# Kernel tuning notes

Hardware: AMD Instinct MI355X
Metric: run time of the kernel (lower is better)

## Reference

```python
import jax, jax.numpy as jnp
import numpy as np

L, B, H, D, S, FF = 24, 4, 16, 512, 4096, 2048
HD = D // H
POS = 2048  # current kv_cache_len (write position)
EPS = 1e-5
SCALE = 1.0 / np.sqrt(HD)


def layer_norm(x, w, b):
    m = jnp.mean(x, axis=-1, keepdims=True)
    v = jnp.mean(jnp.square(x - m), axis=-1, keepdims=True)
    return (x - m) * jax.lax.rsqrt(v + EPS) * w + b


def setup_inputs() -> dict:
    key = jax.random.key(0)
    ks = jax.random.split(key, 12)
    f = lambda k, shape: jax.random.normal(k, shape, dtype=jnp.float32) * 0.02
    # decode mask: positions [0, POS] are attendable (index_fill_ sets POS True)
    attn_mask = jnp.broadcast_to(jnp.arange(S) <= POS, (B, H, 1, S))
    return {
        "x": jax.random.normal(ks[0], (B, 1, D), dtype=jnp.float32),
        "k_cache": jax.random.normal(ks[1], (L, B, H, S, HD), dtype=jnp.float32),
        "v_cache": jax.random.normal(ks[2], (L, B, H, S, HD), dtype=jnp.float32),
        "attn_mask": attn_mask,
        "qkv_w": f(ks[3], (L, 3 * D, D)),
        "qkv_b": f(ks[4], (L, 3 * D)),
        "out_w": f(ks[5], (L, D, D)),
        "out_b": f(ks[6], (L, D)),
        "mlp_w1": f(ks[7], (L, FF, D)),
        "mlp_b1": f(ks[8], (L, FF)),
        "mlp_w2": f(ks[9], (L, D, FF)),
        "mlp_b2": f(ks[10], (L, D)),
        "norm_w1": jnp.ones((L, D), jnp.float32),
        "norm_b1": jnp.zeros((L, D), jnp.float32),
        "norm_w2": jnp.ones((L, D), jnp.float32),
        "norm_b2": jnp.zeros((L, D), jnp.float32),
        "kv_cache_len": POS,
    }


def reference(x, k_cache, v_cache, attn_mask, qkv_w, qkv_b, out_w, out_b,
              mlp_w1, mlp_b1, mlp_w2, mlp_b2, norm_w1, norm_b1, norm_w2,
              norm_b2, kv_cache_len):
    pos = kv_cache_len

    def block(h, p):
        kc0, vc0, qw, qb, ow, ob, w1, b1, w2, b2, nw1, nb1, nw2, nb2 = p
        qkv = h @ qw.T + qb                      # [B,1,3D]
        q, k, v = jnp.split(qkv, 3, axis=-1)
        q = q.reshape(B, 1, H, HD).transpose(0, 2, 1, 3)   # [B,H,1,HD]
        k = k.reshape(B, 1, H, HD).transpose(0, 2, 1, 3)
        v = v.reshape(B, 1, H, HD).transpose(0, 2, 1, 3)
        # in-place cache update at write position (index_copy_ on dim 2)
        kc = kc0.at[:, :, pos, :].set(k[:, :, 0, :])       # [B,H,S,HD]
        vc = vc0.at[:, :, pos, :].set(v[:, :, 0, :])
        scores = jnp.einsum('bhqd,bhkd->bhqk', q, kc) * SCALE
        scores = jnp.where(attn_mask, scores, -1e9)
        attn = jnp.einsum('bhqk,bhkd->bhqd', jax.nn.softmax(scores, axis=-1), vc)
        attn = attn.transpose(0, 2, 1, 3).reshape(B, 1, D)
        attn = attn @ ow.T + ob
        h = layer_norm(h + attn, nw1, nb1)
        mlp = jax.nn.relu(h @ w1.T + b1) @ w2.T + b2
        h = layer_norm(h + mlp, nw2, nb2)
        return h, None

    xs = (k_cache, v_cache, qkv_w, qkv_b, out_w, out_b, mlp_w1, mlp_b1,
          mlp_w2, mlp_b2, norm_w1, norm_b1, norm_w2, norm_b2)
    out, _ = jax.lax.scan(block, x, xs)
    return out
```

## Files before the change

kernel.cpp:

```cpp
#include <hip/hip_runtime.h>


#define DEV __device__ __forceinline__

static constexpr int LNUM = 24;
static constexpr int B = 4;
static constexpr int H = 16;
static constexpr int D = 512;
static constexpr int S = 4096;
static constexpr int FF = 2048;
static constexpr int HD = 32;
static constexpr int NCH = 9;
static constexpr float EPS = 1e-5f;
static constexpr float SCALE = 0.17677669529663687f;

DEV float waveReduceSum(float v) {
#pragma unroll
    for (int o = 32; o > 0; o >>= 1) v += __shfl_xor(v, o);
    return v;
}
DEV float waveReduceMax(float v) {
#pragma unroll
    for (int o = 32; o > 0; o >>= 1) v = fmaxf(v, __shfl_xor(v, o));
    return v;
}
DEV float blockReduceSum(float v, float* red) {
    v = waveReduceSum(v);
    __syncthreads();
    if ((threadIdx.x & 63) == 0) red[threadIdx.x >> 6] = v;
    __syncthreads();
    return red[0] + red[1] + red[2] + red[3];
}
DEV float blockReduceMax(float v, float* red) {
    v = waveReduceMax(v);
    __syncthreads();
    if ((threadIdx.x & 63) == 0) red[threadIdx.x >> 6] = v;
    __syncthreads();
    return fmaxf(fmaxf(red[0], red[1]), fmaxf(red[2], red[3]));
}

__global__ __launch_bounds__(256) void k_qkv(
    const float* __restrict__ hsrc, int apply_ln,
    const float* __restrict__ nw, const float* __restrict__ nb,
    const float* __restrict__ w, const float* __restrict__ bias,
    float* __restrict__ qkv)
{
    const int lane = threadIdx.x & 63;
    const int wid = (blockIdx.x << 2) + (threadIdx.x >> 6);
    const int b = wid / 1536;
    const int r = wid - b * 1536;
    const float* hb = hsrc + (b << 9);
    const int k0 = lane << 3;
    float4 h0 = *(const float4*)(hb + k0);
    float4 h1 = *(const float4*)(hb + k0 + 4);
    float hv[8] = {h0.x, h0.y, h0.z, h0.w, h1.x, h1.y, h1.z, h1.w};
    if (apply_ln) {
        float s = 0.f, s2 = 0.f;
#pragma unroll
        for (int j = 0; j < 8; ++j) { s += hv[j]; s2 += hv[j] * hv[j]; }
        s = waveReduceSum(s);
        s2 = waveReduceSum(s2);
        float mean = s * (1.f / 512.f);
        float var = s2 * (1.f / 512.f) - mean * mean;
        float rs = rsqrtf(var + EPS);
        float4 nw0 = *(const float4*)(nw + k0);
        float4 nw1 = *(const float4*)(nw + k0 + 4);
        float4 nb0 = *(const float4*)(nb + k0);
        float4 nb1 = *(const float4*)(nb + k0 + 4);
        float nwv[8] = {nw0.x, nw0.y, nw0.z, nw0.w, nw1.x, nw1.y, nw1.z, nw1.w};
        float nbv[8] = {nb0.x, nb0.y, nb0.z, nb0.w, nb1.x, nb1.y, nb1.z, nb1.w};
#pragma unroll
        for (int j = 0; j < 8; ++j) hv[j] = (hv[j] - mean) * rs * nwv[j] + nbv[j];
    }
    const float* wr = w + (size_t)r * 512 + k0;
    float4 w0 = *(const float4*)(wr);
    float4 w1 = *(const float4*)(wr + 4);
    float acc = w0.x * hv[0] + w0.y * hv[1] + w0.z * hv[2] + w0.w * hv[3]
              + w1.x * hv[4] + w1.y * hv[5] + w1.z * hv[6] + w1.w * hv[7];
    acc = waveReduceSum(acc);
    if (lane == 0) {
        float v = acc + bias[r];
        if (r < 512) v *= SCALE;
        qkv[b * 1536 + r] = v;
    }
}

__global__ __launch_bounds__(256) void k_attn(
    const float* __restrict__ kc, const float* __restrict__ vc,
    const float* __restrict__ qkv, float* __restrict__ part,
    const int* __restrict__ posp)
{
    const int tid = threadIdx.x;
    const int c = blockIdx.x % NCH;
    const int bh = blockIdx.x / NCH;
    const int b = bh >> 4, h = bh & 15;
    const int pos = posp[0];
    __shared__ float qs[32];
    __shared__ float es[256];
    __shared__ float red[4];
    __shared__ float op[8][33];
    if (tid < 32) qs[tid] = qkv[b * 1536 + h * 32 + tid];
    __syncthreads();
    float score = -1e30f;
    bool act = false;
    if (c < 8) {
        int p = c * 256 + tid;
        act = (p < pos);
        const float4* kp = (const float4*)(kc + ((size_t)bh * S + p) * HD);
        float s = 0.f;
#pragma unroll
        for (int i = 0; i < 8; ++i) {
            float4 kv = kp[i];
            s += qs[4 * i] * kv.x + qs[4 * i + 1] * kv.y + qs[4 * i + 2] * kv.z + qs[4 * i + 3] * kv.w;
        }
        if (act) score = s;
    } else if (tid == 0) {
        act = true;
        const float* kp = qkv + b * 1536 + 512 + h * 32;
        float s = 0.f;
#pragma unroll
        for (int j = 0; j < 32; ++j) s += qs[j] * kp[j];
        score = s;
    }
    float m = blockReduceMax(score, red);
    float e = act ? expf(score - m) : 0.f;
    es[tid] = e;
    float l = blockReduceSum(e, red);
    const int d = tid & 31, g = tid >> 5;
    float acc = 0.f;
    if (c < 8) {
        const float* vp = vc + ((size_t)bh * S + c * 256 + g * 32) * HD + d;
#pragma unroll 8
        for (int i = 0; i < 32; ++i) acc += es[g * 32 + i] * vp[(size_t)i * HD];
    } else if (g == 0) {
        acc = es[0] * qkv[b * 1536 + 1024 + h * 32 + d];
    }
    op[g][d] = acc;
    __syncthreads();
    if (tid < 32) {
        float o = 0.f;
#pragma unroll
        for (int gg = 0; gg < 8; ++gg) o += op[gg][tid];
        float* pp = part + (size_t)(bh * NCH + c) * 34;
        pp[2 + tid] = o;
        if (tid == 0) { pp[0] = m; pp[1] = l; }
    }
}

__global__ __launch_bounds__(256) void k_outproj(
    const float* __restrict__ part,
    const float* __restrict__ ow, const float* __restrict__ ob,
    const float* __restrict__ hsrc, int apply_ln,
    const float* __restrict__ nw, const float* __restrict__ nb,
    float* __restrict__ t1)
{
    const int tid = threadIdx.x;
    const int b = blockIdx.x >> 5;
    const int oc = blockIdx.x & 31;
    __shared__ float attn_s[512];
    __shared__ float hln[512];
    __shared__ float mh[16], sh[16];
    __shared__ float red[4];
    if (tid < 16) {
        const float* pp = part + (size_t)(b * 16 + tid) * NCH * 34;
        float m = -1e30f;
        for (int c = 0; c < NCH; ++c) m = fmaxf(m, pp[c * 34]);
        float ss = 0.f;
        for (int c = 0; c < NCH; ++c) ss += pp[c * 34 + 1] * expf(pp[c * 34] - m);
        mh[tid] = m;
        sh[tid] = ss;
    }
    __syncthreads();
#pragma unroll
    for (int e = tid; e < 512; e += 256) {
        int h = e >> 5, d = e & 31;
        const float* pp = part + (size_t)(b * 16 + h) * NCH * 34;
        float o = 0.f;
        for (int c = 0; c < NCH; ++c) o += pp[c * 34 + 2 + d] * expf(pp[c * 34] - mh[h]);
        attn_s[e] = o / sh[h];
    }
    float a0 = hsrc[(b << 9) + tid], a1 = hsrc[(b << 9) + 256 + tid];
    if (apply_ln) {
        float s = blockReduceSum(a0 + a1, red);
        float s2 = blockReduceSum(a0 * a0 + a1 * a1, red);
        float mean = s * (1.f / 512.f);
        float rs = rsqrtf(s2 * (1.f / 512.f) - mean * mean + EPS);
        hln[tid] = (a0 - mean) * rs * nw[tid] + nb[tid];
        hln[tid + 256] = (a1 - mean) * rs * nw[tid + 256] + nb[tid + 256];
    } else {
        hln[tid] = a0;
        hln[tid + 256] = a1;
    }
    __syncthreads();
    const int w = tid >> 6, lane = tid & 63, k0 = lane << 3;
#pragma unroll
    for (int oi = 0; oi < 4; ++oi) {
        int dd = (oc << 4) + (w << 2) + oi;
        const float4* wp = (const float4*)(ow + (size_t)dd * 512 + k0);
        float4 w0 = wp[0], w1 = wp[1];
        float acc = w0.x * attn_s[k0] + w0.y * attn_s[k0 + 1] + w0.z * attn_s[k0 + 2] + w0.w * attn_s[k0 + 3]
                  + w1.x * attn_s[k0 + 4] + w1.y * attn_s[k0 + 5] + w1.z * attn_s[k0 + 6] + w1.w * attn_s[k0 + 7];
        acc = waveReduceSum(acc);
        if (lane == 0) t1[(b << 9) + dd] = hln[dd] + acc + ob[dd];
    }
}

__global__ __launch_bounds__(256) void k_mlp1(
    const float* __restrict__ t1,
    const float* __restrict__ nw, const float* __restrict__ nb,
    const float* __restrict__ w1, const float* __restrict__ b1,
    float* __restrict__ m1)
{
    const int tid = threadIdx.x;
    const int b = blockIdx.x >> 7;
    const int oc = blockIdx.x & 127;
    __shared__ float hln[512];
    __shared__ float red[4];
    float a0 = t1[(b << 9) + tid], a1 = t1[(b << 9) + 256 + tid];
    float s = blockReduceSum(a0 + a1, red);
    float s2 = blockReduceSum(a0 * a0 + a1 * a1, red);
    float mean = s * (1.f / 512.f);
    float rs = rsqrtf(s2 * (1.f / 512.f) - mean * mean + EPS);
    hln[tid] = (a0 - mean) * rs * nw[tid] + nb[tid];
    hln[tid + 256] = (a1 - mean) * rs * nw[tid + 256] + nb[tid + 256];
    __syncthreads();
    const int w = tid >> 6, lane = tid & 63, k0 = lane << 3;
#pragma unroll
    for (int oi = 0; oi < 4; ++oi) {
        int r = (oc << 4) + (w << 2) + oi;
        const float4* wp = (const float4*)(w1 + (size_t)r * 512 + k0);
        float4 w0 = wp[0], w1v = wp[1];
        float acc = w0.x * hln[k0] + w0.y * hln[k0 + 1] + w0.z * hln[k0 + 2] + w0.w * hln[k0 + 3]
                  + w1v.x * hln[k0 + 4] + w1v.y * hln[k0 + 5] + w1v.z * hln[k0 + 6] + w1v.w * hln[k0 + 7];
        acc = waveReduceSum(acc);
        if (lane == 0) m1[(b << 11) + r] = fmaxf(acc + b1[r], 0.f);
    }
}

__global__ __launch_bounds__(256) void k_mlp2(
    const float* __restrict__ m1, const float* __restrict__ t1,
    const float* __restrict__ nw, const float* __restrict__ nb,
    const float* __restrict__ w2, const float* __restrict__ b2,
    float* __restrict__ sout)
{
    const int tid = threadIdx.x;
    const int b = blockIdx.x >> 7;
    const int oc = blockIdx.x & 127;
    __shared__ float ms[2048];
    __shared__ float red[4];
#pragma unroll
    for (int i = 0; i < 8; ++i) ms[tid + (i << 8)] = m1[(b << 11) + tid + (i << 8)];
    float a0 = t1[(b << 9) + tid], a1 = t1[(b << 9) + 256 + tid];
    float s = blockReduceSum(a0 + a1, red);
    float s2 = blockReduceSum(a0 * a0 + a1 * a1, red);
    float mean = s * (1.f / 512.f);
    float rs = rsqrtf(s2 * (1.f / 512.f) - mean * mean + EPS);
    const int w = tid >> 6, lane = tid & 63;
    const int dd = (oc << 2) + w;
    const float4* wp = (const float4*)(w2 + (size_t)dd * 2048);
    float acc = 0.f;
#pragma unroll
    for (int i = 0; i < 8; ++i) {
        int idx = (i << 6) + lane;
        float4 q = wp[idx];
        int k = idx << 2;
        acc += q.x * ms[k] + q.y * ms[k + 1] + q.z * ms[k + 2] + q.w * ms[k + 3];
    }
    acc = waveReduceSum(acc);
    if (lane == 0) {
        float td = t1[(b << 9) + dd];
        float hd = (td - mean) * rs * nw[dd] + nb[dd];
        sout[(b << 9) + dd] = hd + acc + b2[dd];
    }
}

__global__ __launch_bounds__(256) void k_finalln(
    const float* __restrict__ sbuf,
    const float* __restrict__ nw, const float* __restrict__ nb,
    float* __restrict__ out)
{
    const int b = blockIdx.x, tid = threadIdx.x;
    __shared__ float red[4];
    float a0 = sbuf[(b << 9) + tid], a1 = sbuf[(b << 9) + 256 + tid];
    float s = blockReduceSum(a0 + a1, red);
    float s2 = blockReduceSum(a0 * a0 + a1 * a1, red);
    float mean = s * (1.f / 512.f);
    float rs = rsqrtf(s2 * (1.f / 512.f) - mean * mean + EPS);
    out[(b << 9) + tid] = (a0 - mean) * rs * nw[tid] + nb[tid];
    out[(b << 9) + 256 + tid] = (a1 - mean) * rs * nw[tid + 256] + nb[tid + 256];
}

extern "C" void kernel_launch(void* const* d_in, const int* in_sizes, int n_in,
                              void* d_out, int out_size, void* d_ws, size_t ws_size,
                              hipStream_t stream)
{
    const float* x    = (const float*)d_in[0];
    const float* kc   = (const float*)d_in[1];
    const float* vc   = (const float*)d_in[2];
    const float* qkvw = (const float*)d_in[4];
    const float* qkvb = (const float*)d_in[5];
    const float* outw = (const float*)d_in[6];
    const float* outb = (const float*)d_in[7];
    const float* w1   = (const float*)d_in[8];
    const float* b1   = (const float*)d_in[9];
    const float* w2   = (const float*)d_in[10];
    const float* b2   = (const float*)d_in[11];
    const float* nw1  = (const float*)d_in[12];
    const float* nb1  = (const float*)d_in[13];
    const float* nw2  = (const float*)d_in[14];
    const float* nb2  = (const float*)d_in[15];
    const int*   posp = (const int*)d_in[16];

    float* ws      = (float*)d_ws;
    float* qkvbuf  = ws;
    float* part    = qkvbuf + 6144;
    float* t1      = part + 19584;
    float* m1      = t1 + 2048;
    float* sbuf    = m1 + 8192;

    const size_t kvLayerStride = (size_t)B * H * S * HD;

    for (int l = 0; l < LNUM; ++l) {
        const float* hsrc = (l == 0) ? x : sbuf;
        const int aln = (l > 0) ? 1 : 0;
        const float* pnw = (l > 0) ? (nw2 + (size_t)(l - 1) * 512) : nullptr;
        const float* pnb = (l > 0) ? (nb2 + (size_t)(l - 1) * 512) : nullptr;

        k_qkv<<<1536, 256, 0, stream>>>(hsrc, aln, pnw, pnb,
                                        qkvw + (size_t)l * 1536 * 512,
                                        qkvb + (size_t)l * 1536, qkvbuf);
        k_attn<<<B * H * NCH, 256, 0, stream>>>(kc + (size_t)l * kvLayerStride,
                                                vc + (size_t)l * kvLayerStride,
                                                qkvbuf, part, posp);
        k_outproj<<<B * 32, 256, 0, stream>>>(part,
                                              outw + (size_t)l * 512 * 512,
                                              outb + (size_t)l * 512,
                                              hsrc, aln, pnw, pnb, t1);
        k_mlp1<<<B * 128, 256, 0, stream>>>(t1,
                                            nw1 + (size_t)l * 512, nb1 + (size_t)l * 512,
                                            w1 + (size_t)l * FF * D, b1 + (size_t)l * FF, m1);
        k_mlp2<<<B * 128, 256, 0, stream>>>(m1, t1,
                                            nw1 + (size_t)l * 512, nb1 + (size_t)l * 512,
                                            w2 + (size_t)l * D * FF, b2 + (size_t)l * 512, sbuf);
    }
    k_finalln<<<B, 256, 0, stream>>>(sbuf, nw2 + 23 * 512, nb2 + 23 * 512, (float*)d_out);
}
```

Measured before the change: 820.1 us.

## Fuse all layers into one persistent cooperative kernel with grid syncs

```diff
diff --git a/kernel.cpp b/kernel.cpp
--- a/kernel.cpp
+++ b/kernel.cpp
@@ -1,4 +1,7 @@
 #include <hip/hip_runtime.h>
+#include <hip/hip_cooperative_groups.h>
+
+namespace cg = cooperative_groups;
 
 
 #define DEV __device__ __forceinline__
@@ -24,19 +27,336 @@
     for (int o = 32; o > 0; o >>= 1) v = fmaxf(v, __shfl_xor(v, o));
     return v;
 }
-DEV float blockReduceSum(float v, float* red) {
+DEV float blockReduceSum(float v, volatile float* red) {
     v = waveReduceSum(v);
     __syncthreads();
     if ((threadIdx.x & 63) == 0) red[threadIdx.x >> 6] = v;
     __syncthreads();
     return red[0] + red[1] + red[2] + red[3];
 }
-DEV float blockReduceMax(float v, float* red) {
+DEV float blockReduceMax(float v, volatile float* red) {
     v = waveReduceMax(v);
     __syncthreads();
     if ((threadIdx.x & 63) == 0) red[threadIdx.x >> 6] = v;
     __syncthreads();
     return fmaxf(fmaxf(red[0], red[1]), fmaxf(red[2], red[3]));
+}
+
+struct Params {
+    const float *x, *kc, *vc;
+    const float *qkvw, *qkvb, *outw, *outb, *w1, *b1, *w2, *b2;
+    const float *nw1, *nb1, *nw2, *nb2;
+    const int* posp;
+    float *qkvbuf, *part, *t1, *m1, *sbuf, *out;
+};
+
+__global__ __launch_bounds__(256, 2) void mega(Params p) {
+    cg::grid_group grid = cg::this_grid();
+    const int blk = blockIdx.x;
+    const int tid = threadIdx.x;
+    const int w = tid >> 6;
+    const int lane = tid & 63;
+    const int pos = p.posp[0];
+
+    __shared__ float SM[6160];
+    float* red = SM + 6152;
+
+    for (int l = 0; l < LNUM; ++l) {
+        const float* hsrc = (l == 0) ? p.x : p.sbuf;
+        const bool aln = (l > 0);
+        const float* pnw = p.nw2 + (aln ? (size_t)(l - 1) * 512 : 0);
+        const float* pnb = p.nb2 + (aln ? (size_t)(l - 1) * 512 : 0);
+        const float* qwL = p.qkvw + (size_t)l * 1536 * 512;
+        const float* qbL = p.qkvb + (size_t)l * 1536;
+        const float* kcL = p.kc + (size_t)l * 8388608;
+        const float* vcL = p.vc + (size_t)l * 8388608;
+        const float* owL = p.outw + (size_t)l * 512 * 512;
+        const float* obL = p.outb + (size_t)l * 512;
+        const float* w1L = p.w1 + (size_t)l * 2048 * 512;
+        const float* b1L = p.b1 + (size_t)l * 2048;
+        const float* w2L = p.w2 + (size_t)l * 512 * 2048;
+        const float* b2L = p.b2 + (size_t)l * 512;
+        const float* n1w = p.nw1 + (size_t)l * 512;
+        const float* n1b = p.nb1 + (size_t)l * 512;
+
+        {
+            const float4* s4 = (const float4*)hsrc;
+            float4* m4 = (float4*)SM;
+            m4[tid] = s4[tid];
+            m4[tid + 256] = s4[tid + 256];
+            __syncthreads();
+            float4* h4 = (float4*)(SM + (w << 9));
+            float4 aa = h4[lane], bb = h4[lane + 64];
+            float s = aa.x + aa.y + aa.z + aa.w + bb.x + bb.y + bb.z + bb.w;
+            float s2 = aa.x * aa.x + aa.y * aa.y + aa.z * aa.z + aa.w * aa.w
+                     + bb.x * bb.x + bb.y * bb.y + bb.z * bb.z + bb.w * bb.w;
+            s = waveReduceSum(s);
+            s2 = waveReduceSum(s2);
+            float mean = s * (1.f / 512.f);
+            float rs = rsqrtf(s2 * (1.f / 512.f) - mean * mean + EPS);
+            if (aln) {
+                const float4* gw4 = (const float4*)pnw;
+                const float4* gb4 = (const float4*)pnb;
+                float4 gw = gw4[lane], gb = gb4[lane];
+                aa.x = (aa.x - mean) * rs * gw.x + gb.x;
+                aa.y = (aa.y - mean) * rs * gw.y + gb.y;
+                aa.z = (aa.z - mean) * rs * gw.z + gb.z;
+                aa.w = (aa.w - mean) * rs * gw.w + gb.w;
+                h4[lane] = aa;
+                gw = gw4[lane + 64]; gb = gb4[lane + 64];
+                bb.x = (bb.x - mean) * rs * gw.x + gb.x;
+                bb.y = (bb.y - mean) * rs * gw.y + gb.y;
+                bb.z = (bb.z - mean) * rs * gw.z + gb.z;
+                bb.w = (bb.w - mean) * rs * gw.w + gb.w;
+                h4[lane + 64] = bb;
+            }
+            __syncthreads();
+            const int r = (blk << 2) + w;
+            if (r < 1536) {
+                const float4* wr4 = (const float4*)(qwL + (size_t)r * 512);
+                float4 wA = wr4[lane], wB = wr4[lane + 64];
+                float acc[4];
+#pragma unroll
+                for (int b = 0; b < 4; ++b) {
+                    const float4* hb4 = (const float4*)(SM + (b << 9));
+                    float4 hA = hb4[lane], hB = hb4[lane + 64];
+                    float a = wA.x * hA.x + wA.y * hA.y + wA.z * hA.z + wA.w * hA.w
+                            + wB.x * hB.x + wB.y * hB.y + wB.z * hB.z + wB.w * hB.w;
+                    acc[b] = waveReduceSum(a);
+                }
+                if (lane == 0) {
+                    float bias = qbL[r];
+                    float sc = (r < 512) ? SCALE : 1.f;
+#pragma unroll
+                    for (int b = 0; b < 4; ++b)
+                        p.qkvbuf[b * 1536 + r] = (acc[b] + bias) * sc;
+                }
+            }
+        }
+        grid.sync();
+
+        {
+            const int c = blk & 7, bh = blk >> 3;
+            const int b = bh >> 4, h = bh & 15;
+            float* qs = SM;
+            float* es = SM + 32;
+            float* op = SM + 288;
+            float* sn = SM + 560;
+            if (tid < 32) qs[tid] = p.qkvbuf[b * 1536 + h * 32 + tid];
+            __syncthreads();
+            const int pp = (c << 8) + tid;
+            const bool act = pp < pos;
+            const float4* kp = (const float4*)(kcL + ((size_t)bh * 4096 + pp) * 32);
+            float sc = 0.f;
+#pragma unroll
+            for (int i = 0; i < 8; ++i) {
+                float4 kv = kp[i];
+                sc += qs[4 * i] * kv.x + qs[4 * i + 1] * kv.y
+                    + qs[4 * i + 2] * kv.z + qs[4 * i + 3] * kv.w;
+            }
+            float score = act ? sc : -1e30f;
+            float smax = score;
+            float snew = 0.f;
+            if (c == 7 && tid == 0) {
+                const float* kn = p.qkvbuf + b * 1536 + 512 + h * 32;
+                for (int j = 0; j < 32; ++j) snew += qs[j] * kn[j];
+                smax = fmaxf(smax, snew);
+            }
+            float m = blockReduceMax(smax, red);
+            if (tid == 0) sn[0] = (c == 7) ? expf(snew - m) : 0.f;
+            float e = act ? expf(score - m) : 0.f;
+            es[tid] = e;
+            float lsum = blockReduceSum(e, red) + sn[0];
+            const int d = tid & 31, g = tid >> 5;
+            float acc = 0.f;
+            const float* vp = vcL + ((size_t)bh * 4096 + (c << 8) + (g << 5)) * 32 + d;
+#pragma unroll 8
+            for (int i = 0; i < 32; ++i) acc += es[(g << 5) + i] * vp[(size_t)i * 32];
+            if (g == 0) acc += sn[0] * p.qkvbuf[b * 1536 + 1024 + h * 32 + d];
+            op[g * 33 + d] = acc;
+            __syncthreads();
+            if (tid < 32) {
+                float o = 0.f;
+#pragma unroll
+                for (int gg = 0; gg < 8; ++gg) o += op[gg * 33 + tid];
+                float* pt = p.part + (size_t)((bh << 3) + c) * 34;
+                pt[2 + tid] = o;
+                if (tid == 0) { pt[0] = m; pt[1] = lsum; }
+            }
+        }
+        grid.sync();
+
+        {
+            const float4* s4 = (const float4*)hsrc;
+            float4* m4 = (float4*)SM;
+            m4[tid] = s4[tid];
+            m4[tid + 256] = s4[tid + 256];
+            __syncthreads();
+            float4* h4 = (float4*)(SM + (w << 9));
+            float4 aa = h4[lane], bb = h4[lane + 64];
+            float s = aa.x + aa.y + aa.z + aa.w + bb.x + bb.y + bb.z + bb.w;
+            float s2 = aa.x * aa.x + aa.y * aa.y + aa.z * aa.z + aa.w * aa.w
+                     + bb.x * bb.x + bb.y * bb.y + bb.z * bb.z + bb.w * bb.w;
+            s = waveReduceSum(s);
+            s2 = waveReduceSum(s2);
+            float mean = s * (1.f / 512.f);
+            float rs = rsqrtf(s2 * (1.f / 512.f) - mean * mean + EPS);
+            if (tid < 64) {
+                const float* pt = p.part + (size_t)(tid << 3) * 34;
+                float mh = -1e30f;
+#pragma unroll
+                for (int cc = 0; cc < 8; ++cc) mh = fmaxf(mh, pt[cc * 34]);
+                float ssum = 0.f;
+#pragma unroll
+                for (int cc = 0; cc < 8; ++cc) ssum += pt[cc * 34 + 1] * expf(pt[cc * 34] - mh);
+                SM[2048 + tid] = mh;
+                SM[2112 + tid] = ssum;
+            }
+            __syncthreads();
+#pragma unroll
+            for (int k = 0; k < 8; ++k) {
+                int idx = tid + (k << 8);
+                int b = idx >> 9, e = idx & 511, hh = e >> 5, dd = e & 31;
+                int bh = (b << 4) + hh;
+                const float* pt = p.part + (size_t)(bh << 3) * 34;
+                float mh = SM[2048 + bh];
+                float inv = 1.f / SM[2112 + bh];
+                float o = 0.f;
+#pragma unroll
+                for (int cc = 0; cc < 8; ++cc) o += pt[cc * 34 + 2 + dd] * expf(pt[cc * 34] - mh);
+                SM[2176 + idx] = o * inv;
+            }
+            __syncthreads();
+            const int dd = blk;
+            const float4* wr4 = (const float4*)(owL + (size_t)dd * 512);
+            float4 wA = wr4[lane], wB = wr4[lane + 64];
+            const float4* a4 = (const float4*)(SM + 2176 + (w << 9));
+            float4 hA = a4[lane], hB = a4[lane + 64];
+            float acc = wA.x * hA.x + wA.y * hA.y + wA.z * hA.z + wA.w * hA.w
+                      + wB.x * hB.x + wB.y * hB.y + wB.z * hB.z + wB.w * hB.w;
+            acc = waveReduceSum(acc);
+            if (lane == 0) {
+                float hv = SM[(w << 9) + dd];
+                if (aln) hv = (hv - mean) * rs * pnw[dd] + pnb[dd];
+                p.t1[(w << 9) + dd] = hv + acc + obL[dd];
+            }
+        }
+        grid.sync();
+
+        {
+            const float4* s4 = (const float4*)p.t1;
+            float4* m4 = (float4*)SM;
+            m4[tid] = s4[tid];
+            m4[tid + 256] = s4[tid + 256];
+            __syncthreads();
+            float4* h4 = (float4*)(SM + (w << 9));
+            float4 aa = h4[lane], bb = h4[lane + 64];
+            float s = aa.x + aa.y + aa.z + aa.w + bb.x + bb.y + bb.z + bb.w;
+            float s2 = aa.x * aa.x + aa.y * aa.y + aa.z * aa.z + aa.w * aa.w
+                     + bb.x * bb.x + bb.y * bb.y + bb.z * bb.z + bb.w * bb.w;
+            s = waveReduceSum(s);
+            s2 = waveReduceSum(s2);
+            float mean = s * (1.f / 512.f);
+            float rs = rsqrtf(s2 * (1.f / 512.f) - mean * mean + EPS);
+            {
+                const float4* gw4 = (const float4*)n1w;
+                const float4* gb4 = (const float4*)n1b;
+                float4 gw = gw4[lane], gb = gb4[lane];
+                aa.x = (aa.x - mean) * rs * gw.x + gb.x;
+                aa.y = (aa.y - mean) * rs * gw.y + gb.y;
+                aa.z = (aa.z - mean) * rs * gw.z + gb.z;
+                aa.w = (aa.w - mean) * rs * gw.w + gb.w;
+                h4[lane] = aa;
+                gw = gw4[lane + 64]; gb = gb4[lane + 64];
+                bb.x = (bb.x - mean) * rs * gw.x + gb.x;
+                bb.y = (bb.y - mean) * rs * gw.y + gb.y;
+                bb.z = (bb.z - mean) * rs * gw.z + gb.z;
+                bb.w = (bb.w - mean) * rs * gw.w + gb.w;
+                h4[lane + 64] = bb;
+            }
+            __syncthreads();
+            const int r = (blk << 2) + w;
+            const float4* wr4 = (const float4*)(w1L + (size_t)r * 512);
+            float4 wA = wr4[lane], wB = wr4[lane + 64];
+            float acc[4];
+#pragma unroll
+            for (int b = 0; b < 4; ++b) {
+                const float4* hb4 = (const float4*)(SM + (b << 9));
+                float4 hA = hb4[lane], hB = hb4[lane + 64];
+                float a = wA.x * hA.x + wA.y * hA.y + wA.z * hA.z + wA.w * hA.w
+                        + wB.x * hB.x + wB.y * hB.y + wB.z * hB.z + wB.w * hB.w;
+                acc[b] = waveReduceSum(a);
+            }
+            if (lane == 0) {
+                float bv = b1L[r];
+#pragma unroll
+                for (int b = 0; b < 4; ++b)
+                    p.m1[(b << 11) + r] = fmaxf(acc[b] + bv, 0.f);
+            }
+        }
+        grid.sync();
+
+        {
+            const float4* t4 = (const float4*)p.t1;
+            float4* tB = (float4*)(SM + 4096);
+            tB[tid] = t4[tid];
+            tB[tid + 256] = t4[tid + 256];
+            __syncthreads();
+            const float4* h4 = (const float4*)(SM + 4096 + (w << 9));
+            float4 aa = h4[lane], bb = h4[lane + 64];
+            float s = aa.x + aa.y + aa.z + aa.w + bb.x + bb.y + bb.z + bb.w;
+            float s2 = aa.x * aa.x + aa.y * aa.y + aa.z * aa.z + aa.w * aa.w
+                     + bb.x * bb.x + bb.y * bb.y + bb.z * bb.z + bb.w * bb.w;
+            s = waveReduceSum(s);
+            s2 = waveReduceSum(s2);
+            float mean = s * (1.f / 512.f);
+            float rs = rsqrtf(s2 * (1.f / 512.f) - mean * mean + EPS);
+            const int dd = blk;
+            const float4* wr4 = (const float4*)(w2L + (size_t)dd * 2048);
+            float acc = 0.f;
+#pragma unroll
+            for (int half = 0; half < 2; ++half) {
+                __syncthreads();
+#pragma unroll
+                for (int i = 0; i < 4; ++i) {
+                    int idx = tid + (i << 8);
+                    int b = idx >> 8;
+                    int f = idx & 255;
+                    ((float4*)SM)[idx] =
+                        ((const float4*)(p.m1 + (b << 11) + (half << 10)))[f];
+                }
+                __syncthreads();
+                const float4* mb4 = (const float4*)SM + (w << 8);
+#pragma unroll
+                for (int i = 0; i < 4; ++i) {
+                    float4 q = wr4[(half << 8) + (i << 6) + lane];
+                    float4 mm = mb4[(i << 6) + lane];
+                    acc += q.x * mm.x + q.y * mm.y + q.z * mm.z + q.w * mm.w;
+                }
+            }
+            acc = waveReduceSum(acc);
+            if (lane == 0) {
+                float tv = SM[4096 + (w << 9) + dd];
+                float hv = (tv - mean) * rs * n1w[dd] + n1b[dd];
+                p.sbuf[(w << 9) + dd] = hv + acc + b2L[dd];
+            }
+        }
+        grid.sync();
+    }
+
+    if (blk < 4) {
+        const int b = blk;
+        const float* nw = p.nw2 + 23 * 512;
+        const float* nb = p.nb2 + 23 * 512;
+        float a0 = p.sbuf[(b << 9) + tid];
+        float a1 = p.sbuf[(b << 9) + 256 + tid];
+        float s = blockReduceSum(a0 + a1, red);
+        float s2 = blockReduceSum(a0 * a0 + a1 * a1, red);
+        float mean = s * (1.f / 512.f);
+        float rs = rsqrtf(s2 * (1.f / 512.f) - mean * mean + EPS);
+        p.out[(b << 9) + tid] = (a0 - mean) * rs * nw[tid] + nb[tid];
+        p.out[(b << 9) + 256 + tid] = (a1 - mean) * rs * nw[tid + 256] + nb[tid + 256];
+    }
 }
 
 __global__ __launch_bounds__(256) void k_qkv(
@@ -61,8 +381,7 @@
         s = waveReduceSum(s);
         s2 = waveReduceSum(s2);
         float mean = s * (1.f / 512.f);
-        float var = s2 * (1.f / 512.f) - mean * mean;
-        float rs = rsqrtf(var + EPS);
+        float rs = rsqrtf(s2 * (1.f / 512.f) - mean * mean + EPS);
         float4 nw0 = *(const float4*)(nw + k0);
         float4 nw1 = *(const float4*)(nw + k0 + 4);
         float4 nb0 = *(const float4*)(nb + k0);
@@ -311,13 +630,38 @@
     const float* nb2  = (const float*)d_in[15];
     const int*   posp = (const int*)d_in[16];
 
-    float* ws      = (float*)d_ws;
-    float* qkvbuf  = ws;
-    float* part    = qkvbuf + 6144;
-    float* t1      = part + 19584;
-    float* m1      = t1 + 2048;
-    float* sbuf    = m1 + 8192;
-
+    int dev = 0, cu = 0, nb = 0;
+    hipGetDevice(&dev);
+    hipDeviceGetAttribute(&cu, hipDeviceAttributeMultiprocessorCount, dev);
+    hipOccupancyMaxActiveBlocksPerMultiprocessor(&nb, (const void*)mega, 256, 0);
+    const bool coop_ok = ((long)nb * cu >= 512);
+
+    float* ws = (float*)d_ws;
+
+    if (coop_ok) {
+        Params prm;
+        prm.x = x; prm.kc = kc; prm.vc = vc;
+        prm.qkvw = qkvw; prm.qkvb = qkvb; prm.outw = outw; prm.outb = outb;
+        prm.w1 = w1; prm.b1 = b1; prm.w2 = w2; prm.b2 = b2;
+        prm.nw1 = nw1; prm.nb1 = nb1; prm.nw2 = nw2; prm.nb2 = nb2;
+        prm.posp = posp;
+        prm.qkvbuf = ws;
+        prm.part   = prm.qkvbuf + 6144;
+        prm.t1     = prm.part + 17408;
+        prm.m1     = prm.t1 + 2048;
+        prm.sbuf   = prm.m1 + 8192;
+        prm.out    = (float*)d_out;
+        void* args[] = { &prm };
+        hipLaunchCooperativeKernel(reinterpret_cast<const void*>(&mega),
+                                   dim3(512), dim3(256), args, 0, stream);
+        return;
+    }
+
+    float* qkvbuf = ws;
+    float* part   = qkvbuf + 6144;
+    float* t1     = part + 19584;
+    float* m1     = t1 + 2048;
+    float* sbuf   = m1 + 8192;
     const size_t kvLayerStride = (size_t)B * H * S * HD;
 
     for (int l = 0; l < LNUM; ++l) {
```

Result: slower. 844.5 us (+3.0%).

## Fuse all layers into one persistent cooperative megakernel with per-batch grid barriers

Applied to the files above, without the earlier changes.

```diff
diff --git a/kernel.cpp b/kernel.cpp
--- a/kernel.cpp
+++ b/kernel.cpp
@@ -11,9 +11,12 @@
 static constexpr int FF = 2048;
 static constexpr int HD = 32;
 static constexpr int NCH = 9;
+static constexpr int NBLK = 512;
 static constexpr float EPS = 1e-5f;
 static constexpr float SCALE = 0.17677669529663687f;
 
+DEV float dot4(float4 a, float4 b) { return a.x*b.x + a.y*b.y + a.z*b.z + a.w*b.w; }
+
 DEV float waveReduceSum(float v) {
 #pragma unroll
     for (int o = 32; o > 0; o >>= 1) v += __shfl_xor(v, o);
@@ -24,19 +27,319 @@
     for (int o = 32; o > 0; o >>= 1) v = fmaxf(v, __shfl_xor(v, o));
     return v;
 }
-DEV float blockReduceSum(float v, float* red) {
+DEV float blockReduceSum(float v, volatile float* red) {
     v = waveReduceSum(v);
     __syncthreads();
     if ((threadIdx.x & 63) == 0) red[threadIdx.x >> 6] = v;
     __syncthreads();
     return red[0] + red[1] + red[2] + red[3];
 }
-DEV float blockReduceMax(float v, float* red) {
+DEV float blockReduceMax(float v, volatile float* red) {
     v = waveReduceMax(v);
     __syncthreads();
     if ((threadIdx.x & 63) == 0) red[threadIdx.x >> 6] = v;
     __syncthreads();
     return fmaxf(fmaxf(red[0], red[1]), fmaxf(red[2], red[3]));
+}
+
+DEV void g_arrive(unsigned* sub, unsigned* root, unsigned subTarget) {
+    __syncthreads();
+    if (threadIdx.x == 0) {
+        __builtin_amdgcn_fence(__ATOMIC_RELEASE, "agent");
+        unsigned old = __hip_atomic_fetch_add(sub, 1u, __ATOMIC_RELAXED,
+                                              __HIP_MEMORY_SCOPE_AGENT);
+        if (old == subTarget - 1u)
+            __hip_atomic_fetch_add(root, 1u, __ATOMIC_RELAXED,
+                                   __HIP_MEMORY_SCOPE_AGENT);
+    }
+}
+DEV void g_wait(unsigned* root, unsigned rootTarget) {
+    if (threadIdx.x == 0) {
+        while (__hip_atomic_load(root, __ATOMIC_RELAXED,
+                                 __HIP_MEMORY_SCOPE_AGENT) < rootTarget)
+            __builtin_amdgcn_s_sleep(1);
+    }
+    __syncthreads();
+    __builtin_amdgcn_fence(__ATOMIC_ACQUIRE, "agent");
+}
+
+struct Params {
+    const float *x, *kc, *vc;
+    const float *qkvw, *qkvb, *outw, *outb, *w1, *b1, *w2, *b2;
+    const float *nw1, *nb1, *nw2, *nb2;
+    const int* posp;
+    float *part, *t1, *m1, *sbuf, *out;
+    unsigned* bar;
+};
+
+__global__ __launch_bounds__(256, 2) void mega(Params p) {
+    const int blk = blockIdx.x;
+    const int b = blk >> 7;
+    const int gblk = blk & 127;
+    const int tid = threadIdx.x;
+    const int w = tid >> 6;
+    const int lane = tid & 63;
+    const int pos = p.posp[0];
+
+    __shared__ float SM[2308];
+    float* red = SM + 2304;
+
+    float* partg = p.part + b * 4352;
+    float* t1g   = p.t1 + (b << 9);
+    float* m1g   = p.m1 + (b << 11);
+    float* sbufg = p.sbuf + (b << 9);
+    unsigned* root = p.bar + (size_t)b * 512;
+    unsigned* sub  = root + 32 + (gblk >> 4) * 32;
+    unsigned nb_ = 0;
+
+    const int h = gblk >> 3, c = gblk & 7;
+    const int bh = (b << 4) + h;
+
+    for (int l = 0; l < LNUM; ++l) {
+        const float* hsrc = (l == 0) ? (p.x + (b << 9)) : sbufg;
+        const bool aln = (l > 0);
+        const float* pnw = p.nw2 + (aln ? (size_t)(l - 1) * 512 : 0);
+        const float* pnb = p.nb2 + (aln ? (size_t)(l - 1) * 512 : 0);
+        const float* qwL = p.qkvw + (size_t)l * 1536 * 512;
+        const float* qbL = p.qkvb + (size_t)l * 1536;
+        const float* kcL = p.kc + (size_t)l * 8388608;
+        const float* vcL = p.vc + (size_t)l * 8388608;
+        const float* owL = p.outw + (size_t)l * 512 * 512;
+        const float* obL = p.outb + (size_t)l * 512;
+        const float* w1L = p.w1 + (size_t)l * 2048 * 512;
+        const float* b1L = p.b1 + (size_t)l * 2048;
+        const float* w2L = p.w2 + (size_t)l * 512 * 2048;
+        const float* b2L = p.b2 + (size_t)l * 512;
+        const float* n1w = p.nw1 + (size_t)l * 512;
+        const float* n1b = p.nb1 + (size_t)l * 512;
+
+        {
+            const int pp2 = (c << 8) + tid;
+            float4 kpre[8];
+            {
+                const float4* kp = (const float4*)(kcL + ((size_t)bh * 4096 + pp2) * 32);
+#pragma unroll
+                for (int i = 0; i < 8; ++i) kpre[i] = kp[i];
+            }
+            float vpre[32];
+            {
+                const float* vp = vcL + ((size_t)bh * 4096 + (c << 8) + ((tid >> 5) << 5)) * 32 + (tid & 31);
+#pragma unroll
+                for (int i = 0; i < 32; ++i) vpre[i] = vp[(size_t)i * 32];
+            }
+            if (l) g_wait(root, nb_ * 8);
+
+            float a0 = hsrc[tid], a1 = hsrc[tid + 256];
+            float s = blockReduceSum(a0 + a1, red);
+            float s2 = blockReduceSum(a0 * a0 + a1 * a1, red);
+            float mean = s * (1.f / 512.f);
+            float rs = rsqrtf(s2 * (1.f / 512.f) - mean * mean + EPS);
+            if (aln) {
+                SM[tid] = (a0 - mean) * rs * pnw[tid] + pnb[tid];
+                SM[tid + 256] = (a1 - mean) * rs * pnw[tid + 256] + pnb[tid + 256];
+            } else {
+                SM[tid] = a0;
+                SM[tid + 256] = a1;
+            }
+            __syncthreads();
+
+            const int qd = tid >> 3, s8 = tid & 7;
+            {
+                const float4* wr = (const float4*)(qwL + (size_t)((h << 5) + qd) * 512) + s8 * 16;
+                const float4* hh4 = (const float4*)SM + s8 * 16;
+                float a = 0.f;
+#pragma unroll
+                for (int i = 0; i < 16; ++i) a += dot4(wr[i], hh4[i]);
+                a += __shfl_xor(a, 1); a += __shfl_xor(a, 2); a += __shfl_xor(a, 4);
+                if (s8 == 0) SM[1032 + qd] = (a + qbL[(h << 5) + qd]) * SCALE;
+            }
+            if (c == 7) {
+                {
+                    const float4* wr = (const float4*)(qwL + (size_t)(512 + (h << 5) + qd) * 512) + s8 * 16;
+                    const float4* hh4 = (const float4*)SM + s8 * 16;
+                    float a = 0.f;
+#pragma unroll
+                    for (int i = 0; i < 16; ++i) a += dot4(wr[i], hh4[i]);
+                    a += __shfl_xor(a, 1); a += __shfl_xor(a, 2); a += __shfl_xor(a, 4);
+                    if (s8 == 0) SM[1064 + qd] = a + qbL[512 + (h << 5) + qd];
+                }
+                {
+                    const float4* wr = (const float4*)(qwL + (size_t)(1024 + (h << 5) + qd) * 512) + s8 * 16;
+                    const float4* hh4 = (const float4*)SM + s8 * 16;
+                    float a = 0.f;
+#pragma unroll
+                    for (int i = 0; i < 16; ++i) a += dot4(wr[i], hh4[i]);
+                    a += __shfl_xor(a, 1); a += __shfl_xor(a, 2); a += __shfl_xor(a, 4);
+                    if (s8 == 0) SM[1096 + qd] = a + qbL[1024 + (h << 5) + qd];
+                }
+            }
+            __syncthreads();
+
+            float* qs = SM + 1032;
+            float sc = 0.f;
+#pragma unroll
+            for (int i = 0; i < 8; ++i)
+                sc += qs[4 * i] * kpre[i].x + qs[4 * i + 1] * kpre[i].y
+                    + qs[4 * i + 2] * kpre[i].z + qs[4 * i + 3] * kpre[i].w;
+            const bool act = pp2 < pos;
+            float score = act ? sc : -1e30f;
+            float smax = score, snew = 0.f;
+            if (c == 7 && tid == 0) {
+                for (int j = 0; j < 32; ++j) snew += qs[j] * SM[1064 + j];
+                smax = fmaxf(smax, snew);
+            }
+            float m = blockReduceMax(smax, red);
+            if (tid == 0) SM[1128] = (c == 7) ? expf(snew - m) : 0.f;
+            float e = act ? expf(score - m) : 0.f;
+            SM[512 + tid] = e;
+            float lsum = blockReduceSum(e, red) + SM[1128];
+
+            const int d = tid & 31, g = tid >> 5;
+            float acc = 0.f;
+#pragma unroll
+            for (int i = 0; i < 32; ++i) acc += SM[512 + (g << 5) + i] * vpre[i];
+            if (c == 7 && g == 0) acc += SM[1128] * SM[1096 + d];
+            SM[768 + g * 33 + d] = acc;
+            __syncthreads();
+            if (tid < 32) {
+                float o = 0.f;
+#pragma unroll
+                for (int gg = 0; gg < 8; ++gg) o += SM[768 + gg * 33 + tid];
+                float* pt = partg + (size_t)((h << 3) + c) * 34;
+                pt[2 + tid] = o;
+                if (tid == 0) { pt[0] = m; pt[1] = lsum; }
+            }
+            g_arrive(sub, root, (nb_ + 1) * 16); ++nb_;
+        }
+
+        {
+            const int dd = (gblk << 2) + w;
+            float4 oA, oB;
+            {
+                const float4* wr4 = (const float4*)(owL + (size_t)dd * 512);
+                oA = wr4[lane]; oB = wr4[lane + 64];
+            }
+            float a0 = hsrc[tid], a1 = hsrc[tid + 256];
+            g_wait(root, nb_ * 8);
+
+            if (tid < 16) {
+                const float* pt = partg + (size_t)(tid << 3) * 34;
+                float mh = -1e30f;
+#pragma unroll
+                for (int cc = 0; cc < 8; ++cc) mh = fmaxf(mh, pt[cc * 34]);
+                float ssum = 0.f;
+#pragma unroll
+                for (int cc = 0; cc < 8; ++cc) ssum += pt[cc * 34 + 1] * expf(pt[cc * 34] - mh);
+                SM[512 + tid] = mh;
+                SM[528 + tid] = ssum;
+            }
+            __syncthreads();
+#pragma unroll
+            for (int k = 0; k < 2; ++k) {
+                int e = tid + (k << 8);
+                int h2 = e >> 5, d2 = e & 31;
+                const float* pt = partg + (size_t)(h2 << 3) * 34;
+                float mh = SM[512 + h2];
+                float inv = 1.f / SM[528 + h2];
+                float o = 0.f;
+#pragma unroll
+                for (int cc = 0; cc < 8; ++cc) o += pt[cc * 34 + 2 + d2] * expf(pt[cc * 34] - mh);
+                SM[e] = o * inv;
+            }
+            float s = blockReduceSum(a0 + a1, red);
+            float s2 = blockReduceSum(a0 * a0 + a1 * a1, red);
+            float mean = s * (1.f / 512.f);
+            float rs = rsqrtf(s2 * (1.f / 512.f) - mean * mean + EPS);
+            __syncthreads();
+            const float4* as4 = (const float4*)SM;
+            float acc = dot4(oA, as4[lane]) + dot4(oB, as4[lane + 64]);
+            acc = waveReduceSum(acc);
+            if (lane == 0) {
+                float hv = hsrc[dd];
+                if (aln) hv = (hv - mean) * rs * pnw[dd] + pnb[dd];
+                t1g[dd] = hv + acc + obL[dd];
+            }
+            g_arrive(sub, root, (nb_ + 1) * 16); ++nb_;
+        }
+
+        {
+            const int rr = (gblk << 4) + (tid >> 4);
+            const int s16 = tid & 15;
+            float4 w1pre[8];
+            {
+                const float4* wr = (const float4*)(w1L + (size_t)rr * 512) + s16 * 8;
+#pragma unroll
+                for (int i = 0; i < 8; ++i) w1pre[i] = wr[i];
+            }
+            float g0 = n1w[tid], g1 = n1w[tid + 256];
+            float be0 = n1b[tid], be1 = n1b[tid + 256];
+            float bv = b1L[rr];
+            g_wait(root, nb_ * 8);
+
+            float a0 = t1g[tid], a1 = t1g[tid + 256];
+            float s = blockReduceSum(a0 + a1, red);
+            float s2 = blockReduceSum(a0 * a0 + a1 * a1, red);
+            float mean = s * (1.f / 512.f);
+            float rs = rsqrtf(s2 * (1.f / 512.f) - mean * mean + EPS);
+            SM[tid] = (a0 - mean) * rs * g0 + be0;
+            SM[tid + 256] = (a1 - mean) * rs * g1 + be1;
+            __syncthreads();
+            const float4* hh4 = (const float4*)SM + s16 * 8;
+            float a = 0.f;
+#pragma unroll
+            for (int i = 0; i < 8; ++i) a += dot4(w1pre[i], hh4[i]);
+            a += __shfl_xor(a, 1); a += __shfl_xor(a, 2);
+            a += __shfl_xor(a, 4); a += __shfl_xor(a, 8);
+            if (s16 == 0) m1g[rr] = fmaxf(a + bv, 0.f);
+            g_arrive(sub, root, (nb_ + 1) * 16); ++nb_;
+        }
+
+        {
+            const int dd = (gblk << 2) + w;
+            float4 w2pre[8];
+            {
+                const float4* wr4 = (const float4*)(w2L + (size_t)dd * 2048);
+#pragma unroll
+                for (int i = 0; i < 8; ++i) w2pre[i] = wr4[(i << 6) + lane];
+            }
+            float a0 = t1g[tid], a1 = t1g[tid + 256];
+            float tv = 0.f, gw = 0.f, gb = 0.f, bv = 0.f;
+            if (lane == 0) { tv = t1g[dd]; gw = n1w[dd]; gb = n1b[dd]; bv = b2L[dd]; }
+            g_wait(root, nb_ * 8);
+
+            float4* ms4 = (float4*)SM;
+            const float4* m14 = (const float4*)m1g;
+            ms4[tid] = m14[tid];
+            ms4[tid + 256] = m14[tid + 256];
+            float s = blockReduceSum(a0 + a1, red);
+            float s2 = blockReduceSum(a0 * a0 + a1 * a1, red);
+            float mean = s * (1.f / 512.f);
+            float rs = rsqrtf(s2 * (1.f / 512.f) - mean * mean + EPS);
+            __syncthreads();
+            float acc = 0.f;
+#pragma unroll
+            for (int i = 0; i < 8; ++i) acc += dot4(w2pre[i], ms4[(i << 6) + lane]);
+            acc = waveReduceSum(acc);
+            if (lane == 0) {
+                float hl = (tv - mean) * rs * gw + gb;
+                sbufg[dd] = hl + acc + bv;
+            }
+            g_arrive(sub, root, (nb_ + 1) * 16); ++nb_;
+        }
+    }
+
+    if (gblk == 0) {
+        g_wait(root, nb_ * 8);
+        const float* nw = p.nw2 + 23 * 512;
+        const float* nbv = p.nb2 + 23 * 512;
+        float a0 = sbufg[tid], a1 = sbufg[tid + 256];
+        float s = blockReduceSum(a0 + a1, red);
+        float s2 = blockReduceSum(a0 * a0 + a1 * a1, red);
+        float mean = s * (1.f / 512.f);
+        float rs = rsqrtf(s2 * (1.f / 512.f) - mean * mean + EPS);
+        p.out[(b << 9) + tid] = (a0 - mean) * rs * nw[tid] + nbv[tid];
+        p.out[(b << 9) + 256 + tid] = (a1 - mean) * rs * nw[tid + 256] + nbv[tid + 256];
+    }
 }
 
 __global__ __launch_bounds__(256) void k_qkv(
@@ -61,8 +364,7 @@
         s = waveReduceSum(s);
         s2 = waveReduceSum(s2);
         float mean = s * (1.f / 512.f);
-        float var = s2 * (1.f / 512.f) - mean * mean;
-        float rs = rsqrtf(var + EPS);
+        float rs = rsqrtf(s2 * (1.f / 512.f) - mean * mean + EPS);
         float4 nw0 = *(const float4*)(nw + k0);
         float4 nw1 = *(const float4*)(nw + k0 + 4);
         float4 nb0 = *(const float4*)(nb + k0);
@@ -311,13 +613,39 @@
     const float* nb2  = (const float*)d_in[15];
     const int*   posp = (const int*)d_in[16];
 
-    float* ws      = (float*)d_ws;
-    float* qkvbuf  = ws;
-    float* part    = qkvbuf + 6144;
-    float* t1      = part + 19584;
-    float* m1      = t1 + 2048;
-    float* sbuf    = m1 + 8192;
-
+    int dev = 0, cu = 0, nb = 0;
+    hipGetDevice(&dev);
+    hipDeviceGetAttribute(&cu, hipDeviceAttributeMultiprocessorCount, dev);
+    hipOccupancyMaxActiveBlocksPerMultiprocessor(&nb, (const void*)mega, 256, 0);
+    const bool coop_ok = ((long)nb * cu >= NBLK);
+
+    float* ws = (float*)d_ws;
+
+    if (coop_ok) {
+        Params prm;
+        prm.x = x; prm.kc = kc; prm.vc = vc;
+        prm.qkvw = qkvw; prm.qkvb = qkvb; prm.outw = outw; prm.outb = outb;
+        prm.w1 = w1; prm.b1 = b1; prm.w2 = w2; prm.b2 = b2;
+        prm.nw1 = nw1; prm.nb1 = nb1; prm.nw2 = nw2; prm.nb2 = nb2;
+        prm.posp = posp;
+        prm.part = ws;
+        prm.t1   = prm.part + 17408;
+        prm.m1   = prm.t1 + 2048;
+        prm.sbuf = prm.m1 + 8192;
+        prm.out  = (float*)d_out;
+        prm.bar  = (unsigned*)(ws + 29696);
+        hipMemsetAsync(prm.bar, 0, 8192, stream);
+        void* args[] = { &prm };
+        hipLaunchCooperativeKernel(reinterpret_cast<const void*>(&mega),
+                                   dim3(NBLK), dim3(256), args, 0, stream);
+        return;
+    }
+
+    float* qkvbuf = ws;
+    float* part   = qkvbuf + 6144;
+    float* t1     = part + 19584;
+    float* m1     = t1 + 2048;
+    float* sbuf   = m1 + 8192;
     const size_t kvLayerStride = (size_t)B * H * S * HD;
 
     for (int l = 0; l < LNUM; ++l) {
```

Result: slower. 844.4 us (+3.0%).
